# Optimization experiments

Measured on AMD Instinct MI355X. Metric: run time of the kernel, lower is better.

Reference implementation:

```python
import jax, jax.numpy as jnp
import numpy as np

B, L, DF = 1024, 64, 2048
E, U, V = 256, 512, 32000
BN_EPS = 1e-3  # keras BatchNormalization default epsilon


def setup_inputs() -> dict:
    key = jax.random.key(0)
    ks = jax.random.split(key, 16)
    s = lambda *sh: 1.0 / np.sqrt(sh[0])
    return {
        "tokens": jax.random.randint(ks[0], (B, 1), 0, V),
        "featureMap": jax.random.normal(ks[1], (B, L, DF), jnp.float32),
        "prevState": jax.random.normal(ks[2], (B, U), jnp.float32),
        "emb": jax.random.normal(ks[3], (V, E), jnp.float32) * 0.05,
        "Wu": jax.random.normal(ks[4], (DF, U), jnp.float32) * s(DF),
        "bu": jnp.zeros((U,), jnp.float32),
        "Ww": jax.random.normal(ks[5], (U, U), jnp.float32) * s(U),
        "bw": jnp.zeros((U,), jnp.float32),
        "Wv": jax.random.normal(ks[6], (U, 1), jnp.float32) * s(U),
        "bv": jnp.zeros((1,), jnp.float32),
        "gru_k": jax.random.normal(ks[7], (DF + E, 3 * U), jnp.float32) * s(DF + E),
        "gru_rk": jax.random.normal(ks[8], (U, 3 * U), jnp.float32) * s(U),
        "gru_b": jnp.zeros((2, 3 * U), jnp.float32),
        "W1": jax.random.normal(ks[9], (U, U), jnp.float32) * s(U),
        "b1": jnp.zeros((U,), jnp.float32),
        "gamma": jnp.ones((U,), jnp.float32),
        "beta": jnp.zeros((U,), jnp.float32),
        "mmean": jnp.zeros((U,), jnp.float32),
        "mvar": jnp.ones((U,), jnp.float32),
        "W2": jax.random.normal(ks[10], (U, V), jnp.float32) * s(U),
        "b2": jnp.zeros((V,), jnp.float32),
    }


def reference(tokens, featureMap, prevState, emb, Wu, bu, Ww, bw, Wv, bv,
              gru_k, gru_rk, gru_b, W1, b1, gamma, beta, mmean, mvar, W2, b2):
    u = gru_rk.shape[0]
    # Bahdanau attention: score over L pixel positions
    state = prevState[:, None, :]                                   # [B,1,U]
    score = jnp.tanh(featureMap @ Wu + bu + state @ Ww + bw) @ Wv + bv  # [B,L,1]
    attn = jax.nn.softmax(score, axis=1)                            # [B,L,1]
    ctx = jnp.sum(attn * featureMap, axis=1)                        # [B,DF]
    # embedding lookup + concat context
    ex = emb[tokens]                                                # [B,1,E]
    x = jnp.concatenate([ctx[:, None, :], ex], axis=-1)[:, 0, :]    # [B,DF+E]
    # single-step GRU (keras reset_after=True), initial state = zeros
    xg = x @ gru_k + gru_b[0]                                       # [B,3U]
    rg = gru_b[1]                                                   # h0=0 -> recurrent term is just bias
    z = jax.nn.sigmoid(xg[:, :u] + rg[:u])
    r = jax.nn.sigmoid(xg[:, u:2 * u] + rg[u:2 * u])
    hh = jnp.tanh(xg[:, 2 * u:] + r * rg[2 * u:])
    h = (1.0 - z) * hh                                              # z*h0 + (1-z)*hh, h0=0
    # dense -> dropout(eval: identity) -> batchnorm(inference) -> dense
    y = h @ W1 + b1
    y = (y - mmean) * jax.lax.rsqrt(mvar + BN_EPS) * gamma + beta
    logits = y @ W2 + b2                                            # [B,V]
    return logits, h, attn
```

## Files before the change

kernel.cpp:

```cpp
#include <hip/hip_runtime.h>

typedef unsigned short u16;
typedef unsigned int   u32;
typedef __attribute__((ext_vector_type(8))) short short8;
typedef __attribute__((ext_vector_type(4))) float f32x4;

#define DEV static __device__ __forceinline__

DEV u16 f2bf(float f){
  union { float f; u32 u; } v; v.f = f;
  u32 u = v.u;
  u += 0x7fffu + ((u >> 16) & 1u);
  return (u16)(u >> 16);
}
DEV float sigmoidf_(float x){ return 1.f / (1.f + __expf(-x)); }
DEV float tanh_fast(float x){ float e = __expf(2.f * x); return 1.f - 2.f / (e + 1.f); }

DEV void gload16(const void* g, void* l){
  __builtin_amdgcn_global_load_lds(
      (const __attribute__((address_space(1))) void*)g,
      (__attribute__((address_space(3))) void*)l, 16, 0, 0);
}
DEV f32x4 mfma16(short8 a, short8 b, f32x4 c){
  return __builtin_amdgcn_mfma_f32_16x16x32_bf16(a, b, c, 0, 0, 0);
}

__global__ __launch_bounds__(256) void k_transpose_cvt(
    const float* __restrict__ src, u16* __restrict__ dst, int K, int N){
  __shared__ u16 t[64][72];
  int k0 = blockIdx.x << 6, n0 = blockIdx.y << 6;
  int tid = threadIdx.x;
  int c = tid & 63;
  for (int r = tid >> 6; r < 64; r += 4)
    t[r][c] = f2bf(src[(size_t)(k0 + r) * N + n0 + c]);
  __syncthreads();
  int n = tid >> 2, c0 = (tid & 3) << 4;
  union { u16 s[16]; uint4 q[2]; } pk;
#pragma unroll
  for (int i = 0; i < 16; i++) pk.s[i] = t[c0 + i][n];
  uint4* o = (uint4*)(dst + (size_t)(n0 + n) * K + k0 + c0);
  o[0] = pk.q[0]; o[1] = pk.q[1];
}

__global__ __launch_bounds__(512) void k_q(
    const float* __restrict__ ps, const float* __restrict__ Ww,
    const float* __restrict__ bw, const float* __restrict__ bu,
    float* __restrict__ q){
  __shared__ float psl[8][512];
  int b0 = blockIdx.x << 3;
  int tid = threadIdx.x;
#pragma unroll
  for (int i = 0; i < 8; i++) psl[i][tid] = ps[(size_t)(b0 + i) * 512 + tid];
  __syncthreads();
  float acc[8] = {0,0,0,0,0,0,0,0};
  for (int j = 0; j < 512; j++){
    float w = Ww[(size_t)j * 512 + tid];
#pragma unroll
    for (int i = 0; i < 8; i++) acc[i] = fmaf(psl[i][j], w, acc[i]);
  }
  float bias = bw[tid] + bu[tid];
#pragma unroll
  for (int i = 0; i < 8; i++) q[(size_t)(b0 + i) * 512 + tid] = acc[i] + bias;
}

__global__ __launch_bounds__(256) void k_gather(
    const int* __restrict__ tok, const float* __restrict__ emb, u16* __restrict__ xbf){
  int b = blockIdx.x, e = threadIdx.x;
  int t = tok[b];
  xbf[(size_t)b * 2304 + 2048 + e] = f2bf(emb[(size_t)t * 256 + e]);
}

__global__ __launch_bounds__(512) void k_bnprep(
    const float* __restrict__ gamma, const float* __restrict__ beta,
    const float* __restrict__ mmean, const float* __restrict__ mvar,
    const float* __restrict__ b1, float* __restrict__ bns, float* __restrict__ bno){
  int u = threadIdx.x;
  float sc = gamma[u] * rsqrtf(mvar[u] + 1e-3f);
  bns[u] = sc;
  bno[u] = (b1[u] - mmean[u]) * sc + beta[u];
}

__global__ __launch_bounds__(512) void k_attn(
    const float* __restrict__ fm, const u16* __restrict__ WuT,
    const float* __restrict__ q, const float* __restrict__ Wv,
    float* __restrict__ attn_out, u16* __restrict__ xbf){
  __shared__ __align__(16) u16 Al[64 * 64];
  __shared__ __align__(16) u16 Bl[512 * 64];
  __shared__ float qv[512], wvv[512];
  __shared__ float scoreBuf[8][64];
  __shared__ float attn_s[64];

  int b = blockIdx.x;
  int tid = threadIdx.x, wid = tid >> 6, lane = tid & 63;
  qv[tid] = q[(size_t)b * 512 + tid];
  wvv[tid] = Wv[tid];
  const float* fmb = fm + (size_t)b * (64 * 2048);

  f32x4 acc[4][4];
#pragma unroll
  for (int i = 0; i < 4; i++)
#pragma unroll
    for (int j = 0; j < 4; j++) acc[i][j] = (f32x4){0.f, 0.f, 0.f, 0.f};

  int arow = tid >> 3, ac = tid & 7;
  int asl = ac ^ (arow & 7);

  for (int t = 0; t < 32; t++){
    int k0 = t << 6;
    __syncthreads();
    const float* ga = fmb + (size_t)arow * 2048 + k0 + ac * 8;
    float4 v0 = *(const float4*)ga;
    float4 v1 = *(const float4*)(ga + 4);
    union { u16 s[8]; uint4 q; } pk;
    pk.s[0] = f2bf(v0.x); pk.s[1] = f2bf(v0.y); pk.s[2] = f2bf(v0.z); pk.s[3] = f2bf(v0.w);
    pk.s[4] = f2bf(v1.x); pk.s[5] = f2bf(v1.y); pk.s[6] = f2bf(v1.z); pk.s[7] = f2bf(v1.w);
    *(uint4*)&Al[arow * 64 + asl * 8] = pk.q;
#pragma unroll
    for (int i = 0; i < 8; i++){
      int p = ((wid * 8 + i) << 6) + lane;
      int n = p >> 3, sl = p & 7;
      int sl2 = sl ^ (n & 7);
      gload16(WuT + (size_t)n * 2048 + k0 + sl2 * 8,
              (char*)Bl + (size_t)(wid * 8 + i) * 1024);
    }
    __syncthreads();
#pragma unroll
    for (int kh = 0; kh < 2; kh++){
      short8 af[4], bfr[4];
#pragma unroll
      for (int mi = 0; mi < 4; mi++){
        int r = mi * 16 + (lane & 15);
        af[mi] = *(const short8*)&Al[r * 64 + (((kh << 2) + (lane >> 4)) ^ (r & 7)) * 8];
      }
#pragma unroll
      for (int ni = 0; ni < 4; ni++){
        int nr = wid * 64 + ni * 16 + (lane & 15);
        bfr[ni] = *(const short8*)&Bl[nr * 64 + (((kh << 2) + (lane >> 4)) ^ (nr & 7)) * 8];
      }
#pragma unroll
      for (int mi = 0; mi < 4; mi++)
#pragma unroll
        for (int ni = 0; ni < 4; ni++)
          acc[mi][ni] = mfma16(af[mi], bfr[ni], acc[mi][ni]);
    }
  }

  float part[16];
#pragma unroll
  for (int mi = 0; mi < 4; mi++)
#pragma unroll
    for (int j = 0; j < 4; j++){
      float s = 0.f;
#pragma unroll
      for (int ni = 0; ni < 4; ni++){
        int u = wid * 64 + ni * 16 + (lane & 15);
        s += tanh_fast(acc[mi][ni][j] + qv[u]) * wvv[u];
      }
      part[mi * 4 + j] = s;
    }
#pragma unroll
  for (int i = 0; i < 16; i++){
    part[i] += __shfl_xor(part[i], 1);
    part[i] += __shfl_xor(part[i], 2);
    part[i] += __shfl_xor(part[i], 4);
    part[i] += __shfl_xor(part[i], 8);
  }
  if ((lane & 15) == 0){
    int g = lane >> 4;
#pragma unroll
    for (int mi = 0; mi < 4; mi++)
#pragma unroll
      for (int j = 0; j < 4; j++)
        scoreBuf[wid][mi * 16 + g * 4 + j] = part[mi * 4 + j];
  }
  __syncthreads();
  if (tid < 64){
    float s = 0.f;
#pragma unroll
    for (int w = 0; w < 8; w++) s += scoreBuf[w][tid];
    float mx = s;
#pragma unroll
    for (int m = 32; m >= 1; m >>= 1) mx = fmaxf(mx, __shfl_xor(mx, m));
    float e = __expf(s - mx);
    float sum = e;
#pragma unroll
    for (int m = 32; m >= 1; m >>= 1) sum += __shfl_xor(sum, m);
    float a = e / sum;
    attn_s[tid] = a;
    attn_out[(size_t)b * 64 + tid] = a;
  }
  __syncthreads();
  const float4* fmr = (const float4*)fmb;
  float4 cx = {0.f, 0.f, 0.f, 0.f};
  for (int l = 0; l < 64; l++){
    float a = attn_s[l];
    float4 v = fmr[l * 512 + tid];
    cx.x = fmaf(a, v.x, cx.x); cx.y = fmaf(a, v.y, cx.y);
    cx.z = fmaf(a, v.z, cx.z); cx.w = fmaf(a, v.w, cx.w);
  }
  uint2 o;
  o.x = (u32)f2bf(cx.x) | ((u32)f2bf(cx.y) << 16);
  o.y = (u32)f2bf(cx.z) | ((u32)f2bf(cx.w) << 16);
  *(uint2*)&xbf[(size_t)b * 2304 + tid * 4] = o;
}

template<bool OBF>
__global__ __launch_bounds__(512) void k_gemm(
    const u16* __restrict__ A, const u16* __restrict__ Bt,
    const float* __restrict__ scale, const float* __restrict__ off,
    void* __restrict__ Cout, int K, int N){
  __shared__ __align__(16) u16 Alds[2][128 * 64];
  __shared__ __align__(16) u16 Blds[2][128 * 64];
  int n0 = blockIdx.x << 7, m0 = blockIdx.y << 7;
  int tid = threadIdx.x, wid = tid >> 6, lane = tid & 63;
  int wm = wid >> 2, wn = wid & 3;

  f32x4 acc[4][2];
#pragma unroll
  for (int i = 0; i < 4; i++)
#pragma unroll
    for (int j = 0; j < 2; j++) acc[i][j] = (f32x4){0.f, 0.f, 0.f, 0.f};

  auto stage = [&](int s, int k0){
#pragma unroll
    for (int i = 0; i < 2; i++){
      int p = ((wid * 2 + i) << 6) + lane;
      int row = p >> 3, sl = p & 7, sl2 = sl ^ (row & 7);
      gload16(A  + (size_t)(m0 + row) * K + k0 + sl2 * 8,
              (char*)Alds[s] + (size_t)(wid * 2 + i) * 1024);
      gload16(Bt + (size_t)(n0 + row) * K + k0 + sl2 * 8,
              (char*)Blds[s] + (size_t)(wid * 2 + i) * 1024);
    }
  };

  int nk = K >> 6;
  stage(0, 0);
  __syncthreads();
  int cur = 0;
  for (int t = 0; t < nk; t++){
    if (t + 1 < nk) stage(cur ^ 1, (t + 1) << 6);
#pragma unroll
    for (int kh = 0; kh < 2; kh++){
      short8 af[4], bfr[2];
#pragma unroll
      for (int mi = 0; mi < 4; mi++){
        int r = wm * 64 + mi * 16 + (lane & 15);
        af[mi] = *(const short8*)&Alds[cur][r * 64 + (((kh << 2) + (lane >> 4)) ^ (r & 7)) * 8];
      }
#pragma unroll
      for (int ni = 0; ni < 2; ni++){
        int r = wn * 32 + ni * 16 + (lane & 15);
        bfr[ni] = *(const short8*)&Blds[cur][r * 64 + (((kh << 2) + (lane >> 4)) ^ (r & 7)) * 8];
      }
#pragma unroll
      for (int mi = 0; mi < 4; mi++)
#pragma unroll
        for (int ni = 0; ni < 2; ni++)
          acc[mi][ni] = mfma16(af[mi], bfr[ni], acc[mi][ni]);
    }
    __syncthreads();
    cur ^= 1;
  }
#pragma unroll
  for (int ni = 0; ni < 2; ni++){
    int n = n0 + wn * 32 + ni * 16 + (lane & 15);
    float sc = scale ? scale[n] : 1.f;
    float of = off ? off[n] : 0.f;
#pragma unroll
    for (int mi = 0; mi < 4; mi++)
#pragma unroll
      for (int j = 0; j < 4; j++){
        int m = m0 + wm * 64 + mi * 16 + (lane >> 4) * 4 + j;
        float v = acc[mi][ni][j] * sc + of;
        if (OBF) ((u16*)Cout)[(size_t)m * N + n] = f2bf(v);
        else     ((float*)Cout)[(size_t)m * N + n] = v;
      }
  }
}

__global__ __launch_bounds__(512) void k_gates(
    const float* __restrict__ xg, const float* __restrict__ gru_b,
    float* __restrict__ hout, u16* __restrict__ hbf){
  int b = blockIdx.x, u = threadIdx.x;
  const float* rg = gru_b + 1536;
  size_t base = (size_t)b * 1536;
  float z  = sigmoidf_(xg[base + u]        + rg[u]);
  float r  = sigmoidf_(xg[base + 512 + u]  + rg[512 + u]);
  float hh = tanh_fast(xg[base + 1024 + u] + r * rg[1024 + u]);
  float h = (1.f - z) * hh;
  hout[(size_t)b * 512 + u] = h;
  hbf[(size_t)b * 512 + u] = f2bf(h);
}

extern "C" void kernel_launch(void* const* d_in, const int* in_sizes, int n_in,
                              void* d_out, int out_size, void* d_ws, size_t ws_size,
                              hipStream_t stream){
  const int*   tok   = (const int*)  d_in[0];
  const float* fm    = (const float*)d_in[1];
  const float* ps    = (const float*)d_in[2];
  const float* emb   = (const float*)d_in[3];
  const float* Wu    = (const float*)d_in[4];
  const float* bu    = (const float*)d_in[5];
  const float* Ww    = (const float*)d_in[6];
  const float* bw    = (const float*)d_in[7];
  const float* Wv    = (const float*)d_in[8];
  const float* gru_k = (const float*)d_in[10];
  const float* gru_b = (const float*)d_in[12];
  const float* W1    = (const float*)d_in[13];
  const float* b1    = (const float*)d_in[14];
  const float* gamma = (const float*)d_in[15];
  const float* beta  = (const float*)d_in[16];
  const float* mmean = (const float*)d_in[17];
  const float* mvar  = (const float*)d_in[18];
  const float* W2    = (const float*)d_in[19];
  const float* b2    = (const float*)d_in[20];

  float* logits = (float*)d_out;
  float* hout   = (float*)d_out + 32768000;
  float* attn   = (float*)d_out + 33292288;

  char* ws = (char*)d_ws;
  u16*   WuT = (u16*)  (ws + 0);
  u16*   gkT = (u16*)  (ws + 2097152);
  u16*   W2T = (u16*)  (ws + 9175040);
  u16*   W1T = (u16*)  (ws + 41943040);
  float* qws = (float*)(ws + 42467328);
  u16*   xbf = (u16*)  (ws + 44564480);
  float* xg  = (float*)(ws + 49283072);
  u16*   hbf = (u16*)  (ws + 55574528);
  u16*   ybf = (u16*)  (ws + 56623104);
  float* bns = (float*)(ws + 57671680);
  float* bno = (float*)(ws + 57673728);

  k_transpose_cvt<<<dim3(32, 8),  256, 0, stream>>>(Wu,    WuT, 2048, 512);
  k_transpose_cvt<<<dim3(36, 24), 256, 0, stream>>>(gru_k, gkT, 2304, 1536);
  k_transpose_cvt<<<dim3(8, 500), 256, 0, stream>>>(W2,    W2T, 512,  32000);
  k_transpose_cvt<<<dim3(8, 8),   256, 0, stream>>>(W1,    W1T, 512,  512);
  k_q<<<128, 512, 0, stream>>>(ps, Ww, bw, bu, qws);
  k_gather<<<1024, 256, 0, stream>>>(tok, emb, xbf);
  k_bnprep<<<1, 512, 0, stream>>>(gamma, beta, mmean, mvar, b1, bns, bno);
  k_attn<<<1024, 512, 0, stream>>>(fm, WuT, qws, Wv, attn, xbf);
  k_gemm<false><<<dim3(12, 8), 512, 0, stream>>>(xbf, gkT, nullptr, gru_b, xg, 2304, 1536);
  k_gates<<<1024, 512, 0, stream>>>(xg, gru_b, hout, hbf);
  k_gemm<true><<<dim3(4, 8), 512, 0, stream>>>(hbf, W1T, bns, bno, ybf, 512, 512);
  k_gemm<false><<<dim3(250, 8), 512, 0, stream>>>(ybf, W2T, nullptr, b2, logits, 512, 32000);
}
```

Measured before the change: 515.4 us.

## Double-buffer attention GEMM staging, vectorize transpose loads, widen q batch tile

The attention kernel now double-buffers its A and B tiles in LDS. It prefetches the next k-slice of WuT via global_load_lds and the next featureMap slice into registers while MFMAs run on the current buffer, which drops one barrier per iteration. The transpose kernel reads float4 rows and writes packed bf16 pairs instead of scalar loads. k_q processes 16 batch rows per block instead of 8, with half the blocks. Doubling LDS in k_attn (to roughly 140KB) may reduce occupancy, and k_q now runs on only 64 blocks.

```diff
diff --git a/kernel.cpp b/kernel.cpp
--- a/kernel.cpp
+++ b/kernel.cpp
@@ -30,15 +30,19 @@
   __shared__ u16 t[64][72];
   int k0 = blockIdx.x << 6, n0 = blockIdx.y << 6;
   int tid = threadIdx.x;
-  int c = tid & 63;
-  for (int r = tid >> 6; r < 64; r += 4)
-    t[r][c] = f2bf(src[(size_t)(k0 + r) * N + n0 + c]);
-  __syncthreads();
-  int n = tid >> 2, c0 = (tid & 3) << 4;
+  int r = tid >> 2, c0 = (tid & 3) << 4;
+#pragma unroll
+  for (int i = 0; i < 4; i++){
+    float4 v = *(const float4*)&src[(size_t)(k0 + r) * N + n0 + c0 + i * 4];
+    *(u32*)&t[r][c0 + i * 4 + 0] = (u32)f2bf(v.x) | ((u32)f2bf(v.y) << 16);
+    *(u32*)&t[r][c0 + i * 4 + 2] = (u32)f2bf(v.z) | ((u32)f2bf(v.w) << 16);
+  }
+  __syncthreads();
+  int n = tid >> 2, cc = (tid & 3) << 4;
   union { u16 s[16]; uint4 q[2]; } pk;
 #pragma unroll
-  for (int i = 0; i < 16; i++) pk.s[i] = t[c0 + i][n];
-  uint4* o = (uint4*)(dst + (size_t)(n0 + n) * K + k0 + c0);
+  for (int i = 0; i < 16; i++) pk.s[i] = t[cc + i][n];
+  uint4* o = (uint4*)(dst + (size_t)(n0 + n) * K + k0 + cc);
   o[0] = pk.q[0]; o[1] = pk.q[1];
 }
 
@@ -46,21 +50,23 @@
     const float* __restrict__ ps, const float* __restrict__ Ww,
     const float* __restrict__ bw, const float* __restrict__ bu,
     float* __restrict__ q){
-  __shared__ float psl[8][512];
-  int b0 = blockIdx.x << 3;
+  __shared__ float psl[16][512];
+  int b0 = blockIdx.x << 4;
   int tid = threadIdx.x;
 #pragma unroll
-  for (int i = 0; i < 8; i++) psl[i][tid] = ps[(size_t)(b0 + i) * 512 + tid];
-  __syncthreads();
-  float acc[8] = {0,0,0,0,0,0,0,0};
+  for (int i = 0; i < 16; i++) psl[i][tid] = ps[(size_t)(b0 + i) * 512 + tid];
+  __syncthreads();
+  float acc[16];
+#pragma unroll
+  for (int i = 0; i < 16; i++) acc[i] = 0.f;
   for (int j = 0; j < 512; j++){
     float w = Ww[(size_t)j * 512 + tid];
 #pragma unroll
-    for (int i = 0; i < 8; i++) acc[i] = fmaf(psl[i][j], w, acc[i]);
+    for (int i = 0; i < 16; i++) acc[i] = fmaf(psl[i][j], w, acc[i]);
   }
   float bias = bw[tid] + bu[tid];
 #pragma unroll
-  for (int i = 0; i < 8; i++) q[(size_t)(b0 + i) * 512 + tid] = acc[i] + bias;
+  for (int i = 0; i < 16; i++) q[(size_t)(b0 + i) * 512 + tid] = acc[i] + bias;
 }
 
 __global__ __launch_bounds__(256) void k_gather(
@@ -84,8 +90,8 @@
     const float* __restrict__ fm, const u16* __restrict__ WuT,
     const float* __restrict__ q, const float* __restrict__ Wv,
     float* __restrict__ attn_out, u16* __restrict__ xbf){
-  __shared__ __align__(16) u16 Al[64 * 64];
-  __shared__ __align__(16) u16 Bl[512 * 64];
+  __shared__ __align__(16) u16 Al[2 * 64 * 64];
+  __shared__ __align__(16) u16 Bl[2 * 512 * 64];
   __shared__ float qv[512], wvv[512];
   __shared__ float scoreBuf[8][64];
   __shared__ float attn_s[64];
@@ -104,38 +110,54 @@
 
   int arow = tid >> 3, ac = tid & 7;
   int asl = ac ^ (arow & 7);
-
-  for (int t = 0; t < 32; t++){
-    int k0 = t << 6;
-    __syncthreads();
-    const float* ga = fmb + (size_t)arow * 2048 + k0 + ac * 8;
-    float4 v0 = *(const float4*)ga;
-    float4 v1 = *(const float4*)(ga + 4);
-    union { u16 s[8]; uint4 q; } pk;
-    pk.s[0] = f2bf(v0.x); pk.s[1] = f2bf(v0.y); pk.s[2] = f2bf(v0.z); pk.s[3] = f2bf(v0.w);
-    pk.s[4] = f2bf(v1.x); pk.s[5] = f2bf(v1.y); pk.s[6] = f2bf(v1.z); pk.s[7] = f2bf(v1.w);
-    *(uint4*)&Al[arow * 64 + asl * 8] = pk.q;
+  const float* gaBase = fmb + (size_t)arow * 2048 + ac * 8;
+
+  auto stageB = [&](int buf, int k0){
 #pragma unroll
     for (int i = 0; i < 8; i++){
       int p = ((wid * 8 + i) << 6) + lane;
       int n = p >> 3, sl = p & 7;
       int sl2 = sl ^ (n & 7);
       gload16(WuT + (size_t)n * 2048 + k0 + sl2 * 8,
-              (char*)Bl + (size_t)(wid * 8 + i) * 1024);
-    }
-    __syncthreads();
+              (char*)Bl + (size_t)buf * 65536 + (size_t)(wid * 8 + i) * 1024);
+    }
+  };
+  auto writeA = [&](int buf, float4 v0, float4 v1){
+    union { u16 s[8]; uint4 q; } pk;
+    pk.s[0] = f2bf(v0.x); pk.s[1] = f2bf(v0.y); pk.s[2] = f2bf(v0.z); pk.s[3] = f2bf(v0.w);
+    pk.s[4] = f2bf(v1.x); pk.s[5] = f2bf(v1.y); pk.s[6] = f2bf(v1.z); pk.s[7] = f2bf(v1.w);
+    *(uint4*)&Al[buf * 4096 + arow * 64 + asl * 8] = pk.q;
+  };
+
+  stageB(0, 0);
+  {
+    float4 v0 = *(const float4*)gaBase;
+    float4 v1 = *(const float4*)(gaBase + 4);
+    writeA(0, v0, v1);
+  }
+  __syncthreads();
+
+  int cur = 0;
+  for (int t = 0; t < 32; t++){
+    float4 v0, v1;
+    if (t < 31){
+      stageB(cur ^ 1, (t + 1) << 6);
+      const float* ga = gaBase + ((t + 1) << 6);
+      v0 = *(const float4*)ga;
+      v1 = *(const float4*)(ga + 4);
+    }
 #pragma unroll
     for (int kh = 0; kh < 2; kh++){
       short8 af[4], bfr[4];
 #pragma unroll
       for (int mi = 0; mi < 4; mi++){
         int r = mi * 16 + (lane & 15);
-        af[mi] = *(const short8*)&Al[r * 64 + (((kh << 2) + (lane >> 4)) ^ (r & 7)) * 8];
+        af[mi] = *(const short8*)&Al[cur * 4096 + r * 64 + (((kh << 2) + (lane >> 4)) ^ (r & 7)) * 8];
       }
 #pragma unroll
       for (int ni = 0; ni < 4; ni++){
         int nr = wid * 64 + ni * 16 + (lane & 15);
-        bfr[ni] = *(const short8*)&Bl[nr * 64 + (((kh << 2) + (lane >> 4)) ^ (nr & 7)) * 8];
+        bfr[ni] = *(const short8*)&Bl[cur * 32768 + nr * 64 + (((kh << 2) + (lane >> 4)) ^ (nr & 7)) * 8];
       }
 #pragma unroll
       for (int mi = 0; mi < 4; mi++)
@@ -143,6 +165,9 @@
         for (int ni = 0; ni < 4; ni++)
           acc[mi][ni] = mfma16(af[mi], bfr[ni], acc[mi][ni]);
     }
+    if (t < 31) writeA(cur ^ 1, v0, v1);
+    __syncthreads();
+    cur ^= 1;
   }
 
   float part[16];
@@ -336,7 +361,7 @@
   k_transpose_cvt<<<dim3(36, 24), 256, 0, stream>>>(gru_k, gkT, 2304, 1536);
   k_transpose_cvt<<<dim3(8, 500), 256, 0, stream>>>(W2,    W2T, 512,  32000);
   k_transpose_cvt<<<dim3(8, 8),   256, 0, stream>>>(W1,    W1T, 512,  512);
-  k_q<<<128, 512, 0, stream>>>(ps, Ww, bw, bu, qws);
+  k_q<<<64, 512, 0, stream>>>(ps, Ww, bw, bu, qws);
   k_gather<<<1024, 256, 0, stream>>>(tok, emb, xbf);
   k_bnprep<<<1, 512, 0, stream>>>(gamma, beta, mmean, mvar, b1, bns, bno);
   k_attn<<<1024, 512, 0, stream>>>(fm, WuT, qws, Wv, attn, xbf);
```

New measurement: 626.1 us. +21.5%, slower.
